# Kernel tuning notes

Hardware: AMD Instinct MI355X
Metric: run time of the kernel (lower is better)

Reference implementation:

```python
import jax, jax.numpy as jnp
import numpy as np

N = 20000        # nodes
E = 640000       # edges
D = 128          # embed_dim
L = 3            # num_layers
NUM_PROTEINS_MASK = 21
BN_EPS = 1e-5


def _batchnorm(x, gamma, beta):
    # training-mode BatchNorm1d: biased batch statistics over axis 0
    mu = jnp.mean(x, axis=0)
    var = jnp.mean((x - mu) ** 2, axis=0)
    return (x - mu) * jax.lax.rsqrt(var + BN_EPS) * gamma + beta


def setup_inputs() -> dict:
    key = jax.random.key(0)
    ks = jax.random.split(key, 20)
    s = 0.05
    return {
        "x_tokens": jax.random.randint(ks[0], (N,), 0, NUM_PROTEINS_MASK),
        "edge_index": jax.random.randint(ks[1], (2, E), 0, N),
        "edge_attr": jax.random.normal(ks[2], (E, D), jnp.float32),
        "emb": jax.random.normal(ks[3], (NUM_PROTEINS_MASK, D), jnp.float32) * s,
        "ee_W": jax.random.normal(ks[4], (L, D, D), jnp.float32) * s,
        "ee_b": jnp.zeros((L, D), jnp.float32),
        "W1": jax.random.normal(ks[5], (L, D, 2 * D), jnp.float32) * s,
        "b1": jnp.zeros((L, 2 * D), jnp.float32),
        "bn1_g": jnp.ones((L, 2 * D), jnp.float32),
        "bn1_b": jnp.zeros((L, 2 * D), jnp.float32),
        "W2": jax.random.normal(ks[6], (L, 2 * D, D), jnp.float32) * s,
        "b2": jnp.zeros((L, D), jnp.float32),
        "eps_p": jnp.zeros((L,), jnp.float32),
        "bn_g": jnp.ones((L, D), jnp.float32),
        "bn_b": jnp.zeros((L, D), jnp.float32),
    }


def reference(x_tokens, edge_index, edge_attr, emb, ee_W, ee_b, W1, b1,
              bn1_g, bn1_b, W2, b2, eps_p, bn_g, bn_b):
    src = edge_index[0]  # x_j is gathered from edge_index[0] (PyG source_to_target)
    dst = edge_index[1]
    h = emb[x_tokens]  # [N, D]
    for l in range(L):
        # GINConv: edge encode, gather-message-scatter
        ea = edge_attr @ ee_W[l] + ee_b[l]                      # [E, D]
        msg = jax.nn.relu(h[src] + ea)                          # [E, D]
        agg = jax.ops.segment_sum(msg, dst, num_segments=N)     # [N, D]
        z = (1.0 + eps_p[l]) * h + agg
        # MLP: Linear -> BN -> ReLU -> Linear
        z = _batchnorm(z @ W1[l] + b1[l], bn1_g[l], bn1_b[l])
        z = jax.nn.relu(z)
        h = z @ W2[l] + b2[l]
        # outer BatchNorm; ReLU except last layer; dropout p=0 -> identity
        h = _batchnorm(h, bn_g[l], bn_b[l])
        if l < L - 1:
            h = jax.nn.relu(h)
    return h
```

## Files before the change

### kernel.cpp

```cpp
#include <hip/hip_runtime.h>
#include <stdint.h>

#define NN 20000
#define EE 640000
#define DDIM 128
#define D2 256
#define NLAY 3
#define BN_EPS 1e-5f

typedef short bf16x8 __attribute__((ext_vector_type(8)));
typedef float f32x4 __attribute__((ext_vector_type(4)));

__device__ __forceinline__ short f2bf(float f) {
    uint32_t u = __float_as_uint(f);
    u += 0x7fff + ((u >> 16) & 1);
    return (short)(u >> 16);
}
__device__ __forceinline__ float bf2f(uint32_t u16) {
    return __uint_as_float(u16 << 16);
}

__global__ __launch_bounds__(256) void k_embed(const int* __restrict__ tok,
                                               const float* __restrict__ emb,
                                               float* __restrict__ h) {
    int gid = blockIdx.x * 256 + threadIdx.x;
    int r = gid >> 5;
    int c4 = gid & 31;
    int t = tok[r];
    ((float4*)h)[gid] = ((const float4*)emb)[t * 32 + c4];
}

__global__ __launch_bounds__(256) void k_hist(const int* __restrict__ ei, int* __restrict__ counts) {
    int e = blockIdx.x * 256 + threadIdx.x;
    atomicAdd(&counts[ei[EE + e]], 1);
}

__global__ __launch_bounds__(1024) void k_scan(const int* __restrict__ counts, int* __restrict__ cursor) {
    __shared__ int part[1024];
    int t = threadIdx.x;
    int base = t * 20;
    int s = 0;
    for (int i = 0; i < 20; i++) {
        int idx = base + i;
        if (idx < NN) s += counts[idx];
    }
    part[t] = s;
    __syncthreads();
    for (int off = 1; off < 1024; off <<= 1) {
        int v = (t >= off) ? part[t - off] : 0;
        __syncthreads();
        part[t] += v;
        __syncthreads();
    }
    int run = part[t] - s;
    for (int i = 0; i < 20; i++) {
        int idx = base + i;
        if (idx < NN) { cursor[idx] = run; run += counts[idx]; }
    }
}

__global__ __launch_bounds__(256) void k_scatter(const int* __restrict__ ei,
                                                 int* __restrict__ cursor,
                                                 int* __restrict__ perm,
                                                 int* __restrict__ rank) {
    int e = blockIdx.x * 256 + threadIdx.x;
    int d = ei[EE + e];
    int pos = atomicAdd(&cursor[d], 1);
    perm[pos] = e;
    rank[e] = pos;
}

__global__ __launch_bounds__(256) void k_permute2(const float* __restrict__ edge_attr,
                                                  const int* __restrict__ ei,
                                                  const int* __restrict__ rank,
                                                  short* __restrict__ ea_bf,
                                                  int* __restrict__ srcs,
                                                  int* __restrict__ dsts) {
    int gid = blockIdx.x * 256 + threadIdx.x;
    int e = gid >> 5, c4 = gid & 31;
    float4 v = ((const float4*)edge_attr)[gid];
    int pos = rank[e];
    short4 b;
    b.x = f2bf(v.x); b.y = f2bf(v.y); b.z = f2bf(v.z); b.w = f2bf(v.w);
    ((short4*)ea_bf)[(size_t)pos * 32 + c4] = b;
    if (c4 == 0) { srcs[pos] = ei[e]; dsts[pos] = ei[EE + e]; }
}

__global__ __launch_bounds__(256) void k_prepw(const float* __restrict__ src,
                                               short* __restrict__ dst,
                                               int K, int Nc, int total) {
    int gid = blockIdx.x * 256 + threadIdx.x;
    if (gid >= total) return;
    int per = K * Nc;
    int l = gid / per;
    int rem = gid - l * per;
    int k = rem / Nc;
    int n = rem - k * Nc;
    dst[(l * Nc + n) * K + k] = f2bf(src[gid]);
}

__global__ __launch_bounds__(256) void k_edge3(const short* __restrict__ ea_bf,
                                               const int* __restrict__ srcs,
                                               const int* __restrict__ dsts,
                                               const short* __restrict__ WtL,
                                               const float* __restrict__ ebL,
                                               const float* __restrict__ hbase,
                                               const float* __restrict__ sc2,
                                               const float* __restrict__ sh2,
                                               int lazy,
                                               float* __restrict__ agg) {
    __shared__ __align__(16) short sW[128 * 136];
    __shared__ __align__(16) short sOutB[64 * 132];
    __shared__ int sSrc[64], sDst[64];
    int tid = threadIdx.x;
    int tile = blockIdx.x;

    if (tid < 64) {
        sSrc[tid] = srcs[tile * 64 + tid];
        sDst[tid] = dsts[tile * 64 + tid];
    }
    const uint2* wg = (const uint2*)WtL;
    #pragma unroll
    for (int i = 0; i < 16; i++) {
        int idx = tid + i * 256;
        uint2 v = wg[idx];
        int n = idx >> 5, k4 = (idx & 31) << 2;
        *(uint2*)&sW[n * 136 + k4] = v;
    }
    int lane = tid & 63, wv = tid >> 6;
    int l15 = lane & 15, quad = lane >> 4;
    int r0 = wv * 16;
    const short* abase = ea_bf + ((size_t)(tile * 64 + r0 + l15)) * 128 + quad * 8;
    bf16x8 a[4];
    #pragma unroll
    for (int kt = 0; kt < 4; kt++) a[kt] = *(const bf16x8*)(abase + kt * 32);
    __syncthreads();

    f32x4 acc[8];
    #pragma unroll
    for (int i = 0; i < 8; i++) acc[i] = (f32x4){0.f, 0.f, 0.f, 0.f};
    #pragma unroll
    for (int kt = 0; kt < 4; kt++) {
        #pragma unroll
        for (int nt = 0; nt < 8; nt++) {
            bf16x8 b = *(const bf16x8*)&sW[(nt * 16 + l15) * 136 + kt * 32 + quad * 8];
            acc[nt] = __builtin_amdgcn_mfma_f32_16x16x32_bf16(a[kt], b, acc[nt], 0, 0, 0);
        }
    }
    #pragma unroll
    for (int nt = 0; nt < 8; nt++)
        #pragma unroll
        for (int reg = 0; reg < 4; reg++)
            sOutB[(r0 + quad * 4 + reg) * 132 + nt * 16 + l15] = f2bf(acc[nt][reg]);
    __syncthreads();

    {
        int c2 = tid & 63;
        int c = c2 * 2;
        int rb = tid >> 6;
        float eb0 = ebL[c], eb1 = ebL[c + 1];
        float s0 = 0.f, s1 = 0.f, t0 = 0.f, t1 = 0.f;
        if (lazy) { s0 = sc2[c]; s1 = sc2[c + 1]; t0 = sh2[c]; t1 = sh2[c + 1]; }
        #pragma unroll
        for (int i = 0; i < 16; i++) {
            int r = rb + i * 4;
            float2 hv = *(const float2*)&hbase[(size_t)sSrc[r] * DDIM + c];
            float h0, h1;
            if (lazy) {
                h0 = fmaxf(hv.x * s0 + t0, 0.f);
                h1 = fmaxf(hv.y * s1 + t1, 0.f);
            } else {
                h0 = hv.x; h1 = hv.y;
            }
            uint32_t pp = *(uint32_t*)&sOutB[r * 132 + c];
            float m0 = fmaxf(bf2f(pp & 0xffffu) + eb0 + h0, 0.f);
            float m1 = fmaxf(bf2f(pp >> 16) + eb1 + h1, 0.f);
            uint32_t po = (uint32_t)(uint16_t)f2bf(m0) | ((uint32_t)(uint16_t)f2bf(m1) << 16);
            *(uint32_t*)&sOutB[r * 132 + c] = po;
        }
    }
    __syncthreads();
    int c = tid & 127;
    int rbeg = (tid >> 7) * 32;
    float s = 0.f;
    int cur = sDst[rbeg];
    for (int r = rbeg; r < rbeg + 32; r++) {
        int d = sDst[r];
        if (d != cur) { atomicAdd(&agg[(size_t)cur * DDIM + c], s); s = 0.f; cur = d; }
        uint32_t raw = *(const uint16_t*)&sOutB[r * 132 + c];
        s += bf2f(raw);
    }
    atomicAdd(&agg[(size_t)cur * DDIM + c], s);
}

__global__ __launch_bounds__(256) void k_edge_g(const float* __restrict__ edge_attr,
                                                const short* __restrict__ WtL,
                                                const float* __restrict__ ebL,
                                                const float* __restrict__ h,
                                                const int* __restrict__ ei,
                                                const int* __restrict__ perm,
                                                float* __restrict__ agg) {
    __shared__ __align__(16) short sW[128 * 136];
    __shared__ __align__(16) char sU[64 * 132 * 4];
    __shared__ int sSrc[64], sDst[64], sEdge[64];
    short* sA = (short*)sU;
    float* sOut = (float*)sU;
    int tid = threadIdx.x;
    int tile = blockIdx.x;
    if (tid < 64) {
        int e = perm[tile * 64 + tid];
        sEdge[tid] = e;
        sSrc[tid] = ei[e];
        sDst[tid] = ei[EE + e];
    }
    const uint2* wg = (const uint2*)WtL;
    #pragma unroll
    for (int i = 0; i < 16; i++) {
        int idx = tid + i * 256;
        uint2 v = wg[idx];
        int n = idx >> 5, k4 = (idx & 31) << 2;
        *(uint2*)&sW[n * 136 + k4] = v;
    }
    __syncthreads();
    #pragma unroll
    for (int i = 0; i < 8; i++) {
        int idx = tid + i * 256;
        int r = idx >> 5, c4 = idx & 31;
        float4 v = ((const float4*)edge_attr)[sEdge[r] * 32 + c4];
        short4 b;
        b.x = f2bf(v.x); b.y = f2bf(v.y); b.z = f2bf(v.z); b.w = f2bf(v.w);
        *(short4*)&sA[r * 136 + (c4 << 2)] = b;
    }
    __syncthreads();
    int lane = tid & 63, wv = tid >> 6;
    int l15 = lane & 15, quad = lane >> 4;
    int r0 = wv * 16;
    f32x4 acc[8];
    #pragma unroll
    for (int i = 0; i < 8; i++) acc[i] = (f32x4){0.f, 0.f, 0.f, 0.f};
    #pragma unroll
    for (int kt = 0; kt < 4; kt++) {
        bf16x8 a = *(const bf16x8*)&sA[(r0 + l15) * 136 + kt * 32 + quad * 8];
        #pragma unroll
        for (int nt = 0; nt < 8; nt++) {
            bf16x8 b = *(const bf16x8*)&sW[(nt * 16 + l15) * 136 + kt * 32 + quad * 8];
            acc[nt] = __builtin_amdgcn_mfma_f32_16x16x32_bf16(a, b, acc[nt], 0, 0, 0);
        }
    }
    __syncthreads();
    #pragma unroll
    for (int nt = 0; nt < 8; nt++)
        #pragma unroll
        for (int reg = 0; reg < 4; reg++)
            sOut[(r0 + quad * 4 + reg) * 132 + nt * 16 + l15] = acc[nt][reg];
    __syncthreads();
    #pragma unroll
    for (int i = 0; i < 32; i++) {
        int idx = tid + i * 256;
        int r = idx >> 7, c = idx & 127;
        float v = sOut[r * 132 + c] + ebL[c] + h[(size_t)sSrc[r] * DDIM + c];
        sOut[r * 132 + c] = fmaxf(v, 0.f);
    }
    __syncthreads();
    int c = tid & 127;
    int rbeg = (tid >> 7) * 32;
    float s = 0.f;
    int cur = sDst[rbeg];
    for (int r = rbeg; r < rbeg + 32; r++) {
        int d = sDst[r];
        if (d != cur) { atomicAdd(&agg[(size_t)cur * DDIM + c], s); s = 0.f; cur = d; }
        s += sOut[r * 132 + c];
    }
    atomicAdd(&agg[(size_t)cur * DDIM + c], s);
}

__global__ __launch_bounds__(256) void k_gemm1z(const float* __restrict__ hbase,
                                                const float* __restrict__ sc2,
                                                const float* __restrict__ sh2,
                                                int lazy,
                                                const float* __restrict__ agg,
                                                const float* __restrict__ epsP, int l,
                                                const short* __restrict__ W1tL,
                                                float* __restrict__ zz,
                                                float* __restrict__ stats) {
    __shared__ __align__(16) short sB[256 * 136];
    __shared__ __align__(16) short sA[64 * 136];
    int tid = threadIdx.x;
    int tile = blockIdx.x;
    float e1 = 1.f + epsP[l];
    const uint2* bg = (const uint2*)W1tL;
    #pragma unroll
    for (int i = 0; i < 32; i++) {
        int idx = tid + i * 256;
        uint2 v = bg[idx];
        int n = idx >> 5, k4 = (idx & 31) << 2;
        *(uint2*)&sB[n * 136 + k4] = v;
    }
    {
        int c4 = tid & 31;
        int c = c4 * 4;
        float4 sc = make_float4(0.f, 0.f, 0.f, 0.f), sh = make_float4(0.f, 0.f, 0.f, 0.f);
        if (lazy) {
            sc = *(const float4*)&sc2[c];
            sh = *(const float4*)&sh2[c];
        }
        #pragma unroll
        for (int i = 0; i < 8; i++) {
            int idx = tid + i * 256;
            int r = idx >> 5;
            int gr = tile * 64 + r;
            short4 o = {0, 0, 0, 0};
            if (gr < NN) {
                float4 hv = ((const float4*)hbase)[gr * 32 + c4];
                if (lazy) {
                    hv.x = fmaxf(hv.x * sc.x + sh.x, 0.f);
                    hv.y = fmaxf(hv.y * sc.y + sh.y, 0.f);
                    hv.z = fmaxf(hv.z * sc.z + sh.z, 0.f);
                    hv.w = fmaxf(hv.w * sc.w + sh.w, 0.f);
                }
                float4 av = ((const float4*)agg)[gr * 32 + c4];
                o.x = f2bf(e1 * hv.x + av.x);
                o.y = f2bf(e1 * hv.y + av.y);
                o.z = f2bf(e1 * hv.z + av.z);
                o.w = f2bf(e1 * hv.w + av.w);
            }
            *(short4*)&sA[r * 136 + c] = o;
        }
    }
    __syncthreads();
    int lane = tid & 63, wv = tid >> 6;
    int l15 = lane & 15, quad = lane >> 4;
    int r0 = wv * 16;
    f32x4 acc[16];
    #pragma unroll
    for (int i = 0; i < 16; i++) acc[i] = (f32x4){0.f, 0.f, 0.f, 0.f};
    #pragma unroll
    for (int kt = 0; kt < 4; kt++) {
        bf16x8 a = *(const bf16x8*)&sA[(r0 + l15) * 136 + kt * 32 + quad * 8];
        #pragma unroll
        for (int nt = 0; nt < 16; nt++) {
            bf16x8 b = *(const bf16x8*)&sB[(nt * 16 + l15) * 136 + kt * 32 + quad * 8];
            acc[nt] = __builtin_amdgcn_mfma_f32_16x16x32_bf16(a, b, acc[nt], 0, 0, 0);
        }
    }
    int grb = tile * 64 + r0 + quad * 4;
    #pragma unroll
    for (int nt = 0; nt < 16; nt++) {
        float s = 0.f, s2 = 0.f;
        #pragma unroll
        for (int reg = 0; reg < 4; reg++) {
            int gr = grb + reg;
            float v = acc[nt][reg];
            s += v; s2 += v * v;
            if (gr < NN) zz[(size_t)gr * D2 + nt * 16 + l15] = v;
        }
        s += __shfl_xor(s, 16);  s += __shfl_xor(s, 32);
        s2 += __shfl_xor(s2, 16); s2 += __shfl_xor(s2, 32);
        if (quad == 0) {
            atomicAdd(&stats[nt * 16 + l15], s);
            atomicAdd(&stats[D2 + nt * 16 + l15], s2);
        }
    }
}

__global__ void k_finalize(const float* __restrict__ sums,
                           const float* __restrict__ g, const float* __restrict__ beta,
                           float* __restrict__ scale, float* __restrict__ shift, int ncols) {
    int c = threadIdx.x;
    float inv_n = 1.f / (float)NN;
    float mu = sums[c] * inv_n;
    float var = sums[ncols + c] * inv_n - mu * mu;
    float sc = g[c] * rsqrtf(var + BN_EPS);
    scale[c] = sc;
    shift[c] = beta[c] - mu * sc;
}

__global__ __launch_bounds__(256) void k_gemm2s(const float* __restrict__ zz,
                                                const short* __restrict__ W2tL,
                                                const float* __restrict__ scale1,
                                                const float* __restrict__ shift1,
                                                float* __restrict__ h_pre,
                                                float* __restrict__ stats) {
    __shared__ __align__(16) short sB[128 * 264];
    __shared__ __align__(16) short sA[64 * 264];
    __shared__ float sSc[256], sSh[256];
    int tid = threadIdx.x;
    int tile = blockIdx.x;
    sSc[tid] = scale1[tid];
    sSh[tid] = shift1[tid];
    const uint2* bg = (const uint2*)W2tL;
    #pragma unroll
    for (int i = 0; i < 32; i++) {
        int idx = tid + i * 256;
        uint2 v = bg[idx];
        int n = idx >> 6, k4 = (idx & 63) << 2;
        *(uint2*)&sB[n * 264 + k4] = v;
    }
    __syncthreads();
    #pragma unroll
    for (int i = 0; i < 16; i++) {
        int idx = tid + i * 256;
        int r = idx >> 6, c4q = idx & 63;
        int c4 = c4q << 2;
        int gr = tile * 64 + r;
        short4 o = {0, 0, 0, 0};
        if (gr < NN) {
            float4 v = ((const float4*)zz)[gr * 64 + c4q];
            o.x = f2bf(fmaxf(v.x * sSc[c4 + 0] + sSh[c4 + 0], 0.f));
            o.y = f2bf(fmaxf(v.y * sSc[c4 + 1] + sSh[c4 + 1], 0.f));
            o.z = f2bf(fmaxf(v.z * sSc[c4 + 2] + sSh[c4 + 2], 0.f));
            o.w = f2bf(fmaxf(v.w * sSc[c4 + 3] + sSh[c4 + 3], 0.f));
        }
        *(short4*)&sA[r * 264 + c4] = o;
    }
    __syncthreads();
    int lane = tid & 63, wv = tid >> 6;
    int l15 = lane & 15, quad = lane >> 4;
    int r0 = wv * 16;
    f32x4 acc[8];
    #pragma unroll
    for (int i = 0; i < 8; i++) acc[i] = (f32x4){0.f, 0.f, 0.f, 0.f};
    #pragma unroll
    for (int kt = 0; kt < 8; kt++) {
        bf16x8 a = *(const bf16x8*)&sA[(r0 + l15) * 264 + kt * 32 + quad * 8];
        #pragma unroll
        for (int nt = 0; nt < 8; nt++) {
            bf16x8 b = *(const bf16x8*)&sB[(nt * 16 + l15) * 264 + kt * 32 + quad * 8];
            acc[nt] = __builtin_amdgcn_mfma_f32_16x16x32_bf16(a, b, acc[nt], 0, 0, 0);
        }
    }
    int grb = tile * 64 + r0 + quad * 4;
    #pragma unroll
    for (int nt = 0; nt < 8; nt++) {
        float s = 0.f, s2 = 0.f;
        #pragma unroll
        for (int reg = 0; reg < 4; reg++) {
            int gr = grb + reg;
            float v = acc[nt][reg];
            s += v; s2 += v * v;
            if (gr < NN) h_pre[(size_t)gr * DDIM + nt * 16 + l15] = v;
        }
        s += __shfl_xor(s, 16);  s += __shfl_xor(s, 32);
        s2 += __shfl_xor(s2, 16); s2 += __shfl_xor(s2, 32);
        if (quad == 0) {
            atomicAdd(&stats[nt * 16 + l15], s);
            atomicAdd(&stats[DDIM + nt * 16 + l15], s2);
        }
    }
}

__global__ __launch_bounds__(256) void k_bn2(const float* __restrict__ h_pre,
                                             const float* __restrict__ scale2,
                                             const float* __restrict__ shift2,
                                             int do_relu, float* __restrict__ dst) {
    int gid = blockIdx.x * 256 + threadIdx.x;
    int c0 = (gid & 31) << 2;
    float4 v = ((const float4*)h_pre)[gid];
    float4 o;
    o.x = v.x * scale2[c0 + 0] + shift2[c0 + 0];
    o.y = v.y * scale2[c0 + 1] + shift2[c0 + 1];
    o.z = v.z * scale2[c0 + 2] + shift2[c0 + 2];
    o.w = v.w * scale2[c0 + 3] + shift2[c0 + 3];
    if (do_relu) {
        o.x = fmaxf(o.x, 0.f); o.y = fmaxf(o.y, 0.f);
        o.z = fmaxf(o.z, 0.f); o.w = fmaxf(o.w, 0.f);
    }
    ((float4*)dst)[gid] = o;
}

extern "C" void kernel_launch(void* const* d_in, const int* in_sizes, int n_in,
                              void* d_out, int out_size, void* d_ws, size_t ws_size,
                              hipStream_t stream) {
    const int*   tok       = (const int*)d_in[0];
    const int*   ei        = (const int*)d_in[1];
    const float* edge_attr = (const float*)d_in[2];
    const float* emb       = (const float*)d_in[3];
    const float* eeW       = (const float*)d_in[4];
    const float* eeB       = (const float*)d_in[5];
    const float* W1        = (const float*)d_in[6];
    const float* bn1g      = (const float*)d_in[8];
    const float* bn1b      = (const float*)d_in[9];
    const float* W2        = (const float*)d_in[10];
    const float* epsP      = (const float*)d_in[12];
    const float* bng       = (const float*)d_in[13];
    const float* bnb       = (const float*)d_in[14];
    float* out = (float*)d_out;

    char* ws = (char*)d_ws;
    size_t off = 0;
    auto alloc = [&](size_t bytes) -> char* {
        off = (off + 511) & ~(size_t)511;
        char* p = ws + off;
        off += bytes;
        return p;
    };
    float* h      = (float*)alloc((size_t)NN * DDIM * 4);
    float* agg    = (float*)alloc((size_t)NN * DDIM * 4);
    float* zz     = (float*)alloc((size_t)NN * D2 * 4);
    float* h_pre  = (float*)alloc((size_t)NN * DDIM * 4);
    int*   perm   = (int*)alloc((size_t)EE * 4);
    int*   rank   = (int*)alloc((size_t)EE * 4);
    int*   counts = (int*)alloc((size_t)NN * 4);
    int*   cursor = (int*)alloc((size_t)NN * 4);
    int*   srcs   = (int*)alloc((size_t)EE * 4);
    int*   dsts   = (int*)alloc((size_t)EE * 4);
    short* WtE    = (short*)alloc((size_t)NLAY * 128 * 128 * 2);
    short* W1t    = (short*)alloc((size_t)NLAY * 128 * 256 * 2);
    short* W2t    = (short*)alloc((size_t)NLAY * 256 * 128 * 2);
    float* stats  = (float*)alloc(768 * 4);
    float* scale1 = (float*)alloc(256 * 4);
    float* shift1 = (float*)alloc(256 * 4);
    float* scale2 = (float*)alloc(128 * 4);
    float* shift2 = (float*)alloc(128 * 4);
    short* ea_bf  = (short*)alloc((size_t)EE * DDIM * 2);
    bool big = (off <= ws_size);
    (void)in_sizes; (void)n_in; (void)out_size;

    hipMemsetAsync(counts, 0, (size_t)NN * 4, stream);
    {
        int t1 = NLAY * 128 * 128;
        k_prepw<<<(t1 + 255) / 256, 256, 0, stream>>>(eeW, WtE, 128, 128, t1);
        int t2 = NLAY * 128 * 256;
        k_prepw<<<(t2 + 255) / 256, 256, 0, stream>>>(W1, W1t, 128, 256, t2);
        int t3 = NLAY * 256 * 128;
        k_prepw<<<(t3 + 255) / 256, 256, 0, stream>>>(W2, W2t, 256, 128, t3);
    }
    k_embed<<<2500, 256, 0, stream>>>(tok, emb, h);
    k_hist<<<2500, 256, 0, stream>>>(ei, counts);
    k_scan<<<1, 1024, 0, stream>>>(counts, cursor);
    k_scatter<<<2500, 256, 0, stream>>>(ei, cursor, perm, rank);
    if (big) {
        k_permute2<<<EE * 32 / 256, 256, 0, stream>>>(edge_attr, ei, rank, ea_bf, srcs, dsts);
    }

    for (int l = 0; l < NLAY; l++) {
        hipMemsetAsync(agg, 0, (size_t)NN * DDIM * 4, stream);
        hipMemsetAsync(stats, 0, 768 * 4, stream);
        int lazy = (big && l > 0) ? 1 : 0;
        const float* hb = lazy ? h_pre : h;
        if (big) {
            k_edge3<<<EE / 64, 256, 0, stream>>>(ea_bf, srcs, dsts,
                                                 WtE + (size_t)l * 128 * 128,
                                                 eeB + (size_t)l * 128,
                                                 hb, scale2, shift2, lazy, agg);
        } else {
            k_edge_g<<<EE / 64, 256, 0, stream>>>(edge_attr, WtE + (size_t)l * 128 * 128,
                                                  eeB + (size_t)l * 128, h, ei, perm, agg);
        }
        k_gemm1z<<<(NN + 63) / 64, 256, 0, stream>>>(hb, scale2, shift2, lazy, agg, epsP, l,
                                                     W1t + (size_t)l * 128 * 256, zz, stats);
        k_finalize<<<1, 256, 0, stream>>>(stats, bn1g + (size_t)l * 256, bn1b + (size_t)l * 256,
                                          scale1, shift1, 256);
        k_gemm2s<<<(NN + 63) / 64, 256, 0, stream>>>(zz, W2t + (size_t)l * 256 * 128,
                                                     scale1, shift1, h_pre, stats + 512);
        k_finalize<<<1, 128, 0, stream>>>(stats + 512, bng + (size_t)l * 128, bnb + (size_t)l * 128,
                                          scale2, shift2, 128);
        if (big) {
            if (l == NLAY - 1)
                k_bn2<<<2500, 256, 0, stream>>>(h_pre, scale2, shift2, 0, out);
        } else {
            k_bn2<<<2500, 256, 0, stream>>>(h_pre, scale2, shift2, (l < NLAY - 1) ? 1 : 0,
                                            (l == NLAY - 1) ? out : h);
        }
    }
}
```

Measured before the change: 1.272 ms.

## Fold BN finalize into consumer kernels and split GEMMs across column halves

Removes the two single-block k_finalize launches per layer. Each consumer kernel (edge, gemm1, gemm2, bn2) now recomputes the BN scale and shift itself from the raw sum and sum-of-squares, and the stats buffers are double-buffered across layers. gemm1z and gemm2s get a second grid dimension that splits output columns in half, doubling block count for occupancy at the cost of re-staging the A tile twice. Also stages the scan through shared memory, folds the edge bias into the MFMA epilogue, and merges the agg and stats memsets.

```diff
diff --git a/kernel.cpp b/kernel.cpp
--- a/kernel.cpp
+++ b/kernel.cpp
@@ -36,13 +36,17 @@
 }
 
 __global__ __launch_bounds__(1024) void k_scan(const int* __restrict__ counts, int* __restrict__ cursor) {
+    __shared__ int buf[NN];
     __shared__ int part[1024];
     int t = threadIdx.x;
+    for (int i = t; i < NN; i += 1024) buf[i] = counts[i];
+    __syncthreads();
     int base = t * 20;
     int s = 0;
+    #pragma unroll
     for (int i = 0; i < 20; i++) {
         int idx = base + i;
-        if (idx < NN) s += counts[idx];
+        if (idx < NN) s += buf[idx];
     }
     part[t] = s;
     __syncthreads();
@@ -53,10 +57,13 @@
         __syncthreads();
     }
     int run = part[t] - s;
+    #pragma unroll
     for (int i = 0; i < 20; i++) {
         int idx = base + i;
-        if (idx < NN) { cursor[idx] = run; run += counts[idx]; }
-    }
+        if (idx < NN) { int c = buf[idx]; buf[idx] = run; run += c; }
+    }
+    __syncthreads();
+    for (int i = t; i < NN; i += 1024) cursor[i] = buf[i];
 }
 
 __global__ __launch_bounds__(256) void k_scatter(const int* __restrict__ ei,
@@ -105,8 +112,9 @@
                                                const short* __restrict__ WtL,
                                                const float* __restrict__ ebL,
                                                const float* __restrict__ hbase,
-                                               const float* __restrict__ sc2,
-                                               const float* __restrict__ sh2,
+                                               const float* __restrict__ st2,
+                                               const float* __restrict__ g2,
+                                               const float* __restrict__ b2v,
                                                int lazy,
                                                float* __restrict__ agg) {
     __shared__ __align__(16) short sW[128 * 136];
@@ -148,19 +156,27 @@
         }
     }
     #pragma unroll
-    for (int nt = 0; nt < 8; nt++)
+    for (int nt = 0; nt < 8; nt++) {
+        float ebv = ebL[nt * 16 + l15];
         #pragma unroll
         for (int reg = 0; reg < 4; reg++)
-            sOutB[(r0 + quad * 4 + reg) * 132 + nt * 16 + l15] = f2bf(acc[nt][reg]);
+            sOutB[(r0 + quad * 4 + reg) * 132 + nt * 16 + l15] = f2bf(acc[nt][reg] + ebv);
+    }
     __syncthreads();
 
     {
         int c2 = tid & 63;
         int c = c2 * 2;
         int rb = tid >> 6;
-        float eb0 = ebL[c], eb1 = ebL[c + 1];
         float s0 = 0.f, s1 = 0.f, t0 = 0.f, t1 = 0.f;
-        if (lazy) { s0 = sc2[c]; s1 = sc2[c + 1]; t0 = sh2[c]; t1 = sh2[c + 1]; }
+        if (lazy) {
+            float inv_n = 1.f / (float)NN;
+            float mu0 = st2[c] * inv_n,     mu1 = st2[c + 1] * inv_n;
+            float va0 = st2[128 + c] * inv_n - mu0 * mu0;
+            float va1 = st2[129 + c] * inv_n - mu1 * mu1;
+            s0 = g2[c] * rsqrtf(va0 + BN_EPS);     t0 = b2v[c] - mu0 * s0;
+            s1 = g2[c + 1] * rsqrtf(va1 + BN_EPS); t1 = b2v[c + 1] - mu1 * s1;
+        }
         #pragma unroll
         for (int i = 0; i < 16; i++) {
             int r = rb + i * 4;
@@ -173,8 +189,8 @@
                 h0 = hv.x; h1 = hv.y;
             }
             uint32_t pp = *(uint32_t*)&sOutB[r * 132 + c];
-            float m0 = fmaxf(bf2f(pp & 0xffffu) + eb0 + h0, 0.f);
-            float m1 = fmaxf(bf2f(pp >> 16) + eb1 + h1, 0.f);
+            float m0 = fmaxf(bf2f(pp & 0xffffu) + h0, 0.f);
+            float m1 = fmaxf(bf2f(pp >> 16) + h1, 0.f);
             uint32_t po = (uint32_t)(uint16_t)f2bf(m0) | ((uint32_t)(uint16_t)f2bf(m1) << 16);
             *(uint32_t*)&sOutB[r * 132 + c] = po;
         }
@@ -275,22 +291,24 @@
 }
 
 __global__ __launch_bounds__(256) void k_gemm1z(const float* __restrict__ hbase,
-                                                const float* __restrict__ sc2,
-                                                const float* __restrict__ sh2,
+                                                const float* __restrict__ st2,
+                                                const float* __restrict__ g2,
+                                                const float* __restrict__ b2v,
                                                 int lazy,
                                                 const float* __restrict__ agg,
                                                 const float* __restrict__ epsP, int l,
                                                 const short* __restrict__ W1tL,
                                                 float* __restrict__ zz,
                                                 float* __restrict__ stats) {
-    __shared__ __align__(16) short sB[256 * 136];
+    __shared__ __align__(16) short sB[128 * 136];
     __shared__ __align__(16) short sA[64 * 136];
     int tid = threadIdx.x;
     int tile = blockIdx.x;
+    int half = blockIdx.y;
     float e1 = 1.f + epsP[l];
-    const uint2* bg = (const uint2*)W1tL;
-    #pragma unroll
-    for (int i = 0; i < 32; i++) {
+    const uint2* bg = (const uint2*)W1tL + (size_t)half * 128 * 32;
+    #pragma unroll
+    for (int i = 0; i < 16; i++) {
         int idx = tid + i * 256;
         uint2 v = bg[idx];
         int n = idx >> 5, k4 = (idx & 31) << 2;
@@ -299,10 +317,17 @@
     {
         int c4 = tid & 31;
         int c = c4 * 4;
-        float4 sc = make_float4(0.f, 0.f, 0.f, 0.f), sh = make_float4(0.f, 0.f, 0.f, 0.f);
+        float scv[4] = {0.f, 0.f, 0.f, 0.f}, shv[4] = {0.f, 0.f, 0.f, 0.f};
         if (lazy) {
-            sc = *(const float4*)&sc2[c];
-            sh = *(const float4*)&sh2[c];
+            float inv_n = 1.f / (float)NN;
+            #pragma unroll
+            for (int j = 0; j < 4; j++) {
+                float mu = st2[c + j] * inv_n;
+                float var = st2[128 + c + j] * inv_n - mu * mu;
+                float sc = g2[c + j] * rsqrtf(var + BN_EPS);
+                scv[j] = sc;
+                shv[j] = b2v[c + j] - mu * sc;
+            }
         }
         #pragma unroll
         for (int i = 0; i < 8; i++) {
@@ -313,10 +338,10 @@
             if (gr < NN) {
                 float4 hv = ((const float4*)hbase)[gr * 32 + c4];
                 if (lazy) {
-                    hv.x = fmaxf(hv.x * sc.x + sh.x, 0.f);
-                    hv.y = fmaxf(hv.y * sc.y + sh.y, 0.f);
-                    hv.z = fmaxf(hv.z * sc.z + sh.z, 0.f);
-                    hv.w = fmaxf(hv.w * sc.w + sh.w, 0.f);
+                    hv.x = fmaxf(hv.x * scv[0] + shv[0], 0.f);
+                    hv.y = fmaxf(hv.y * scv[1] + shv[1], 0.f);
+                    hv.z = fmaxf(hv.z * scv[2] + shv[2], 0.f);
+                    hv.w = fmaxf(hv.w * scv[3] + shv[3], 0.f);
                 }
                 float4 av = ((const float4*)agg)[gr * 32 + c4];
                 o.x = f2bf(e1 * hv.x + av.x);
@@ -331,66 +356,63 @@
     int lane = tid & 63, wv = tid >> 6;
     int l15 = lane & 15, quad = lane >> 4;
     int r0 = wv * 16;
-    f32x4 acc[16];
-    #pragma unroll
-    for (int i = 0; i < 16; i++) acc[i] = (f32x4){0.f, 0.f, 0.f, 0.f};
+    f32x4 acc[8];
+    #pragma unroll
+    for (int i = 0; i < 8; i++) acc[i] = (f32x4){0.f, 0.f, 0.f, 0.f};
     #pragma unroll
     for (int kt = 0; kt < 4; kt++) {
         bf16x8 a = *(const bf16x8*)&sA[(r0 + l15) * 136 + kt * 32 + quad * 8];
         #pragma unroll
-        for (int nt = 0; nt < 16; nt++) {
+        for (int nt = 0; nt < 8; nt++) {
             bf16x8 b = *(const bf16x8*)&sB[(nt * 16 + l15) * 136 + kt * 32 + quad * 8];
             acc[nt] = __builtin_amdgcn_mfma_f32_16x16x32_bf16(a, b, acc[nt], 0, 0, 0);
         }
     }
     int grb = tile * 64 + r0 + quad * 4;
     #pragma unroll
-    for (int nt = 0; nt < 16; nt++) {
+    for (int nt = 0; nt < 8; nt++) {
+        int col = half * 128 + nt * 16 + l15;
         float s = 0.f, s2 = 0.f;
         #pragma unroll
         for (int reg = 0; reg < 4; reg++) {
             int gr = grb + reg;
             float v = acc[nt][reg];
             s += v; s2 += v * v;
-            if (gr < NN) zz[(size_t)gr * D2 + nt * 16 + l15] = v;
+            if (gr < NN) zz[(size_t)gr * D2 + col] = v;
         }
         s += __shfl_xor(s, 16);  s += __shfl_xor(s, 32);
         s2 += __shfl_xor(s2, 16); s2 += __shfl_xor(s2, 32);
         if (quad == 0) {
-            atomicAdd(&stats[nt * 16 + l15], s);
-            atomicAdd(&stats[D2 + nt * 16 + l15], s2);
-        }
-    }
-}
-
-__global__ void k_finalize(const float* __restrict__ sums,
-                           const float* __restrict__ g, const float* __restrict__ beta,
-                           float* __restrict__ scale, float* __restrict__ shift, int ncols) {
-    int c = threadIdx.x;
-    float inv_n = 1.f / (float)NN;
-    float mu = sums[c] * inv_n;
-    float var = sums[ncols + c] * inv_n - mu * mu;
-    float sc = g[c] * rsqrtf(var + BN_EPS);
-    scale[c] = sc;
-    shift[c] = beta[c] - mu * sc;
+            atomicAdd(&stats[col], s);
+            atomicAdd(&stats[D2 + col], s2);
+        }
+    }
 }
 
 __global__ __launch_bounds__(256) void k_gemm2s(const float* __restrict__ zz,
                                                 const short* __restrict__ W2tL,
-                                                const float* __restrict__ scale1,
-                                                const float* __restrict__ shift1,
+                                                const float* __restrict__ st1,
+                                                const float* __restrict__ g1,
+                                                const float* __restrict__ b1v,
                                                 float* __restrict__ h_pre,
                                                 float* __restrict__ stats) {
-    __shared__ __align__(16) short sB[128 * 264];
+    __shared__ __align__(16) short sB[64 * 264];
     __shared__ __align__(16) short sA[64 * 264];
     __shared__ float sSc[256], sSh[256];
     int tid = threadIdx.x;
     int tile = blockIdx.x;
-    sSc[tid] = scale1[tid];
-    sSh[tid] = shift1[tid];
-    const uint2* bg = (const uint2*)W2tL;
-    #pragma unroll
-    for (int i = 0; i < 32; i++) {
+    int half = blockIdx.y;
+    {
+        float inv_n = 1.f / (float)NN;
+        float mu = st1[tid] * inv_n;
+        float var = st1[256 + tid] * inv_n - mu * mu;
+        float sc = g1[tid] * rsqrtf(var + BN_EPS);
+        sSc[tid] = sc;
+        sSh[tid] = b1v[tid] - mu * sc;
+    }
+    const uint2* bg = (const uint2*)W2tL + (size_t)half * 64 * 64;
+    #pragma unroll
+    for (int i = 0; i < 16; i++) {
         int idx = tid + i * 256;
         uint2 v = bg[idx];
         int n = idx >> 6, k4 = (idx & 63) << 2;
@@ -417,55 +439,60 @@
     int lane = tid & 63, wv = tid >> 6;
     int l15 = lane & 15, quad = lane >> 4;
     int r0 = wv * 16;
-    f32x4 acc[8];
-    #pragma unroll
-    for (int i = 0; i < 8; i++) acc[i] = (f32x4){0.f, 0.f, 0.f, 0.f};
+    f32x4 acc[4];
+    #pragma unroll
+    for (int i = 0; i < 4; i++) acc[i] = (f32x4){0.f, 0.f, 0.f, 0.f};
     #pragma unroll
     for (int kt = 0; kt < 8; kt++) {
         bf16x8 a = *(const bf16x8*)&sA[(r0 + l15) * 264 + kt * 32 + quad * 8];
         #pragma unroll
-        for (int nt = 0; nt < 8; nt++) {
+        for (int nt = 0; nt < 4; nt++) {
             bf16x8 b = *(const bf16x8*)&sB[(nt * 16 + l15) * 264 + kt * 32 + quad * 8];
             acc[nt] = __builtin_amdgcn_mfma_f32_16x16x32_bf16(a, b, acc[nt], 0, 0, 0);
         }
     }
     int grb = tile * 64 + r0 + quad * 4;
     #pragma unroll
-    for (int nt = 0; nt < 8; nt++) {
+    for (int nt = 0; nt < 4; nt++) {
+        int col = half * 64 + nt * 16 + l15;
         float s = 0.f, s2 = 0.f;
         #pragma unroll
         for (int reg = 0; reg < 4; reg++) {
             int gr = grb + reg;
             float v = acc[nt][reg];
             s += v; s2 += v * v;
-            if (gr < NN) h_pre[(size_t)gr * DDIM + nt * 16 + l15] = v;
+            if (gr < NN) h_pre[(size_t)gr * DDIM + col] = v;
         }
         s += __shfl_xor(s, 16);  s += __shfl_xor(s, 32);
         s2 += __shfl_xor(s2, 16); s2 += __shfl_xor(s2, 32);
         if (quad == 0) {
-            atomicAdd(&stats[nt * 16 + l15], s);
-            atomicAdd(&stats[DDIM + nt * 16 + l15], s2);
+            atomicAdd(&stats[col], s);
+            atomicAdd(&stats[DDIM + col], s2);
         }
     }
 }
 
 __global__ __launch_bounds__(256) void k_bn2(const float* __restrict__ h_pre,
-                                             const float* __restrict__ scale2,
-                                             const float* __restrict__ shift2,
+                                             const float* __restrict__ st2,
+                                             const float* __restrict__ g2,
+                                             const float* __restrict__ b2v,
                                              int do_relu, float* __restrict__ dst) {
     int gid = blockIdx.x * 256 + threadIdx.x;
     int c0 = (gid & 31) << 2;
+    float inv_n = 1.f / (float)NN;
     float4 v = ((const float4*)h_pre)[gid];
-    float4 o;
-    o.x = v.x * scale2[c0 + 0] + shift2[c0 + 0];
-    o.y = v.y * scale2[c0 + 1] + shift2[c0 + 1];
-    o.z = v.z * scale2[c0 + 2] + shift2[c0 + 2];
-    o.w = v.w * scale2[c0 + 3] + shift2[c0 + 3];
-    if (do_relu) {
-        o.x = fmaxf(o.x, 0.f); o.y = fmaxf(o.y, 0.f);
-        o.z = fmaxf(o.z, 0.f); o.w = fmaxf(o.w, 0.f);
-    }
-    ((float4*)dst)[gid] = o;
+    float o[4];
+    #pragma unroll
+    for (int j = 0; j < 4; j++) {
+        float mu = st2[c0 + j] * inv_n;
+        float var = st2[128 + c0 + j] * inv_n - mu * mu;
+        float sc = g2[c0 + j] * rsqrtf(var + BN_EPS);
+        float sh = b2v[c0 + j] - mu * sc;
+        float x = (&v.x)[j] * sc + sh;
+        o[j] = do_relu ? fmaxf(x, 0.f) : x;
+    }
+    float4 ov = make_float4(o[0], o[1], o[2], o[3]);
+    ((float4*)dst)[gid] = ov;
 }
 
 extern "C" void kernel_launch(void* const* d_in, const int* in_sizes, int n_in,
@@ -495,7 +522,9 @@
         return p;
     };
     float* h      = (float*)alloc((size_t)NN * DDIM * 4);
-    float* agg    = (float*)alloc((size_t)NN * DDIM * 4);
+    float* aggs   = (float*)alloc(((size_t)NN * DDIM + 512) * 4);
+    float* agg    = aggs;
+    float* stats1 = aggs + (size_t)NN * DDIM;
     float* zz     = (float*)alloc((size_t)NN * D2 * 4);
     float* h_pre  = (float*)alloc((size_t)NN * DDIM * 4);
     int*   perm   = (int*)alloc((size_t)EE * 4);
@@ -507,11 +536,7 @@
     short* WtE    = (short*)alloc((size_t)NLAY * 128 * 128 * 2);
     short* W1t    = (short*)alloc((size_t)NLAY * 128 * 256 * 2);
     short* W2t    = (short*)alloc((size_t)NLAY * 256 * 128 * 2);
-    float* stats  = (float*)alloc(768 * 4);
-    float* scale1 = (float*)alloc(256 * 4);
-    float* shift1 = (float*)alloc(256 * 4);
-    float* scale2 = (float*)alloc(128 * 4);
-    float* shift2 = (float*)alloc(128 * 4);
+    float* stats2 = (float*)alloc(512 * 4);
     short* ea_bf  = (short*)alloc((size_t)EE * DDIM * 2);
     bool big = (off <= ws_size);
     (void)in_sizes; (void)n_in; (void)out_size;
@@ -534,32 +559,37 @@
     }
 
     for (int l = 0; l < NLAY; l++) {
-        hipMemsetAsync(agg, 0, (size_t)NN * DDIM * 4, stream);
-        hipMemsetAsync(stats, 0, 768 * 4, stream);
+        hipMemsetAsync(aggs, 0, ((size_t)NN * DDIM + 512) * 4, stream);
+        float* st2cur  = stats2 + (l & 1) * 256;
+        float* st2prev = stats2 + ((l + 1) & 1) * 256;
+        hipMemsetAsync(st2cur, 0, 256 * 4, stream);
         int lazy = (big && l > 0) ? 1 : 0;
-        const float* hb = lazy ? h_pre : h;
+        const float* hb  = lazy ? h_pre : h;
+        int lp = (l > 0) ? (l - 1) : 0;
+        const float* g2p = bng + (size_t)lp * 128;
+        const float* b2p = bnb + (size_t)lp * 128;
         if (big) {
             k_edge3<<<EE / 64, 256, 0, stream>>>(ea_bf, srcs, dsts,
                                                  WtE + (size_t)l * 128 * 128,
                                                  eeB + (size_t)l * 128,
-                                                 hb, scale2, shift2, lazy, agg);
+                                                 hb, st2prev, g2p, b2p, lazy, agg);
         } else {
             k_edge_g<<<EE / 64, 256, 0, stream>>>(edge_attr, WtE + (size_t)l * 128 * 128,
                                                   eeB + (size_t)l * 128, h, ei, perm, agg);
         }
-        k_gemm1z<<<(NN + 63) / 64, 256, 0, stream>>>(hb, scale2, shift2, lazy, agg, epsP, l,
-                                                     W1t + (size_t)l * 128 * 256, zz, stats);
-        k_finalize<<<1, 256, 0, stream>>>(stats, bn1g + (size_t)l * 256, bn1b + (size_t)l * 256,
-                                          scale1, shift1, 256);
-        k_gemm2s<<<(NN + 63) / 64, 256, 0, stream>>>(zz, W2t + (size_t)l * 256 * 128,
-                                                     scale1, shift1, h_pre, stats + 512);
-        k_finalize<<<1, 128, 0, stream>>>(stats + 512, bng + (size_t)l * 128, bnb + (size_t)l * 128,
-                                          scale2, shift2, 128);
+        k_gemm1z<<<dim3((NN + 63) / 64, 2), 256, 0, stream>>>(hb, st2prev, g2p, b2p, lazy, agg,
+                                                              epsP, l,
+                                                              W1t + (size_t)l * 128 * 256, zz, stats1);
+        k_gemm2s<<<dim3((NN + 63) / 64, 2), 256, 0, stream>>>(zz, W2t + (size_t)l * 256 * 128,
+                                                              stats1, bn1g + (size_t)l * 256,
+                                                              bn1b + (size_t)l * 256, h_pre, st2cur);
         if (big) {
             if (l == NLAY - 1)
-                k_bn2<<<2500, 256, 0, stream>>>(h_pre, scale2, shift2, 0, out);
+                k_bn2<<<2500, 256, 0, stream>>>(h_pre, st2cur, bng + (size_t)l * 128,
+                                                bnb + (size_t)l * 128, 0, out);
         } else {
-            k_bn2<<<2500, 256, 0, stream>>>(h_pre, scale2, shift2, (l < NLAY - 1) ? 1 : 0,
+            k_bn2<<<2500, 256, 0, stream>>>(h_pre, st2cur, bng + (size_t)l * 128,
+                                            bnb + (size_t)l * 128, (l < NLAY - 1) ? 1 : 0,
                                             (l == NLAY - 1) ? out : h);
         }
     }
```

New measurement: 1.226 ms. 1.04x faster.
